# Optimization experiments

Hardware: AMD Instinct MI355X
Metric: run time of the kernel (lower is better)

Reference implementation:

```python
import jax, jax.numpy as jnp
import numpy as np

NUM_CLASSES = 4
SMOOTH = 1e-05
W_DICE, W_CE, W_BOUND = 1.0, 1.0, 0.01
BIG = 1e8  # effectively-infinite squared distance


def _edt_sq_pass(f, axis):
    # Exact 1D squared-distance transform along `axis` via min-plus:
    # out[i] = min_j f[j] + (i-j)^2  (brute-force O(n^2), fully vectorized)
    n = f.shape[axis]
    i = jnp.arange(n, dtype=f.dtype)
    d2 = (i[:, None] - i[None, :]) ** 2  # [n, n]
    fm = jnp.moveaxis(f, axis, -1)
    out = jnp.min(fm[..., None, :] + d2, axis=-1)
    return jnp.moveaxis(out, -1, axis)


def _edt(zero_mask):
    # Euclidean distance to the nearest True voxel of zero_mask
    # (equivalent to scipy distance_transform_edt(~zero_mask)'s convention:
    #  distance to nearest zero of the input == nearest True of zero_mask).
    f = jnp.where(zero_mask, 0.0, BIG).astype(jnp.float32)
    for ax in range(f.ndim):
        f = _edt_sq_pass(f, ax)
    return jnp.sqrt(f)


def _signed_distance(mask):
    # mask: bool [D,H,W]; signed distance map: + outside, - inside.
    d_out = _edt(mask)            # distance(1 - mask)
    d_in = _edt(~mask)            # distance(mask)
    sdf = d_out - d_in
    total = jnp.sum(mask)
    size = mask.size
    sdf = jnp.where(total == 0, jnp.ones_like(sdf), sdf)
    sdf = jnp.where(total == size, -jnp.ones_like(sdf), sdf)
    return sdf


def setup_inputs() -> dict:
    key = jax.random.key(0)
    k1, k2 = jax.random.split(key)
    preds = jax.random.normal(k1, (4, NUM_CLASSES, 64, 64, 64), dtype=jnp.float32)
    targets = jax.random.randint(k2, (4, 64, 64, 64), 0, NUM_CLASSES, dtype=jnp.int32)
    return {"preds": preds, "targets": targets}


def reference(preds, targets):
    B = preds.shape[0]
    probs = jax.nn.softmax(preds, axis=1)  # [B,C,D,H,W]

    # --- Soft Dice ---
    onehot = jax.nn.one_hot(targets, NUM_CLASSES, dtype=preds.dtype)  # [B,D,H,W,C]
    onehot = jnp.moveaxis(onehot, -1, 1)  # [B,C,D,H,W]
    inter = jnp.sum(probs * onehot, axis=(2, 3, 4))
    union = jnp.sum(probs, axis=(2, 3, 4)) + jnp.sum(onehot, axis=(2, 3, 4))
    dice = (2.0 * inter + SMOOTH) / (union + SMOOTH)
    l_dice = 1.0 - jnp.mean(dice)

    # --- Cross entropy (mean over all voxels) ---
    logp = jax.nn.log_softmax(preds, axis=1)
    picked = jnp.take_along_axis(logp, targets[:, None].astype(jnp.int32), axis=1)
    l_ce = -jnp.mean(picked)

    # --- Boundary loss (classes 1..C-1) ---
    l_bound = jnp.float32(0.0)
    for c in range(1, NUM_CLASSES):
        mask_c = targets == c  # [B,D,H,W]
        sdf_c = jax.vmap(_signed_distance)(mask_c)  # [B,D,H,W]
        l_bound = l_bound + jnp.sum(jnp.mean(sdf_c * probs[:, c], axis=(1, 2, 3)))
    l_bound = l_bound / (B * (NUM_CLASSES - 1))

    return W_DICE * l_dice + W_CE * l_ce + W_BOUND * l_bound
```

## Files before the change

kernel.cpp:

```cpp
#include <hip/hip_runtime.h>
#include <hip/hip_bf16.h>
#include <math.h>

#define NVOX 262144
#define BIGF 1e8f

__device__ __forceinline__ unsigned short f2bf(float x) {
    __hip_bfloat16 h = __float2bfloat16(x);
    return *reinterpret_cast<unsigned short*>(&h);
}
__device__ __forceinline__ float bf2f(unsigned short u) {
    __hip_bfloat16 h = *reinterpret_cast<__hip_bfloat16*>(&u);
    return __bfloat162float(h);
}
__device__ __forceinline__ unsigned short dist2_u16(unsigned long long mask, int w) {
    if (mask == 0ull) return 0xFFFFu;
    unsigned long long mr = mask >> w;
    unsigned long long ml = mask << (63 - w);
    int dr = mr ? __builtin_ctzll(mr) : 127;
    int dl = ml ? __builtin_clzll(ml) : 127;
    int dd = dr < dl ? dr : dl;
    return (unsigned short)(dd * dd);
}

__global__ __launch_bounds__(512) void k1_stats_edt1(
    const float* __restrict__ preds, const int* __restrict__ targets,
    unsigned short* __restrict__ bufA, unsigned short* __restrict__ probsT,
    float* __restrict__ part_stats) {
    __shared__ int tgt[64 * 65];
    __shared__ unsigned short tiles[3 * 64 * 65];
    __shared__ float sred[8 * 13];

    int blk = blockIdx.x;
    int b = blk >> 6, d = blk & 63;
    int t = threadIdx.x, lane = t & 63, wid = t >> 6;
    size_t tbase = (size_t)b * NVOX + (size_t)d * 4096;
    size_t pbase = (size_t)(b * 4) * NVOX + (size_t)d * 4096;

    float q[13];
    #pragma unroll
    for (int k = 0; k < 13; ++k) q[k] = 0.0f;

    for (int i = 0; i < 8; ++i) {
        int e = t + 512 * i;
        int h = e >> 6, w = e & 63;
        int tv = targets[tbase + e];
        tgt[h * 65 + w] = tv;
        float x0 = preds[pbase + e];
        float x1 = preds[pbase + NVOX + e];
        float x2 = preds[pbase + 2 * NVOX + e];
        float x3 = preds[pbase + 3 * NVOX + e];
        float m  = fmaxf(fmaxf(x0, x1), fmaxf(x2, x3));
        float e0 = expf(x0 - m), e1 = expf(x1 - m), e2 = expf(x2 - m), e3 = expf(x3 - m);
        float ssum = e0 + e1 + e2 + e3;
        float inv  = 1.0f / ssum;
        float p0 = e0 * inv, p1 = e1 * inv, p2 = e2 * inv, p3 = e3 * inv;
        float xt = (tv == 0) ? x0 : (tv == 1) ? x1 : (tv == 2) ? x2 : x3;
        q[12] += -(xt - m - logf(ssum));
        q[4] += p0; q[5] += p1; q[6] += p2; q[7] += p3;
        if (tv == 0)      { q[0] += p0; q[8]  += 1.0f; }
        else if (tv == 1) { q[1] += p1; q[9]  += 1.0f; }
        else if (tv == 2) { q[2] += p2; q[10] += 1.0f; }
        else              { q[3] += p3; q[11] += 1.0f; }
        int li = h * 65 + w;
        tiles[li]            = f2bf(p1);
        tiles[4160 + li]     = f2bf(p2);
        tiles[2 * 4160 + li] = f2bf(p3);
    }

    #pragma unroll
    for (int k = 0; k < 13; ++k) {
        float x = q[k];
        #pragma unroll
        for (int o = 32; o > 0; o >>= 1) x += __shfl_down(x, o);
        if (lane == 0) sred[wid * 13 + k] = x;
    }
    __syncthreads();
    if (t < 13) {
        float s = 0.0f;
        for (int j = 0; j < 8; ++j) s += sred[j * 13 + t];
        part_stats[t * 256 + blk] = s;
    }

    for (int c = 0; c < 3; ++c) {
        size_t obase = (size_t)(b * 3 + c) * NVOX + (size_t)d * 64;
        for (int w = wid; w < 64; w += 8)
            probsT[obase + (size_t)w * 4096 + lane] = tiles[c * 4160 + lane * 65 + w];
    }
    __syncthreads();

    unsigned short* tA = tiles;
    unsigned short* tB = tiles + 4160;
    for (int c = 1; c <= 3; ++c) {
        for (int r = 0; r < 8; ++r) {
            int row = wid * 8 + r;
            int tv = tgt[row * 65 + lane];
            unsigned long long mask = __ballot(tv == c);
            tA[row * 65 + lane] = dist2_u16(mask, lane);
            tB[row * 65 + lane] = dist2_u16(~mask, lane);
        }
        __syncthreads();
        int combo = b * 3 + c - 1;
        size_t oA = (size_t)combo * NVOX + (size_t)d * 64;
        size_t oB = (size_t)(combo + 12) * NVOX + (size_t)d * 64;
        for (int w = wid; w < 64; w += 8) {
            bufA[oA + (size_t)w * 4096 + lane] = tA[lane * 65 + w];
            bufA[oB + (size_t)w * 4096 + lane] = tB[lane * 65 + w];
        }
        __syncthreads();
    }
}

__global__ __launch_bounds__(512) void k2_edt23_sdf(
    const unsigned short* __restrict__ bufA, const unsigned short* __restrict__ probsT,
    float* __restrict__ part_bound) {
    __shared__ float pl[2][64 * 65];
    __shared__ float sredb[8];
    int blk = blockIdx.x;
    int combo = blk >> 6, w = blk & 63;
    int t = threadIdx.x, lane = t & 63, wid = t >> 6;

    for (int v = 0; v < 2; ++v) {
        const unsigned short* src = bufA + (size_t)(combo + 12 * v) * NVOX + (size_t)w * 4096;
        for (int i = 0; i < 8; ++i) {
            int e = t + 512 * i;
            unsigned short u = src[e];
            pl[v][e + (e >> 6)] = (u == 0xFFFFu) ? BIGF : (float)u;
        }
    }
    __syncthreads();

    for (int v = 0; v < 2; ++v) {
        for (int r = 0; r < 8; ++r) {
            int dd_ = wid * 8 + r;
            float* row = &pl[v][dd_ * 65];
            float best = row[lane];
            for (int dk = 1; dk < 64; ++dk) {
                float d2 = (float)(dk * dk);
                if (__all(d2 >= best)) break;
                int hl = lane - dk; hl = hl < 0 ? 0 : hl;
                int hr = lane + dk; hr = hr > 63 ? 63 : hr;
                best = fminf(fminf(best, row[hl] + d2), row[hr] + d2);
            }
            row[lane] = best;
        }
    }
    __syncthreads();
    for (int v = 0; v < 2; ++v) {
        for (int r = 0; r < 8; ++r) {
            int h = wid * 8 + r;
            float* col = &pl[v][h];
            float best = col[lane * 65];
            for (int dk = 1; dk < 64; ++dk) {
                float d2 = (float)(dk * dk);
                if (__all(d2 >= best)) break;
                int dl = lane - dk; dl = dl < 0 ? 0 : dl;
                int dr = lane + dk; dr = dr > 63 ? 63 : dr;
                best = fminf(fminf(best, col[dl * 65] + d2), col[dr * 65] + d2);
            }
            col[lane * 65] = best;
        }
    }
    __syncthreads();

    const unsigned short* pp = probsT + (size_t)combo * NVOX + (size_t)w * 4096;
    float acc = 0.0f;
    for (int i = 0; i < 8; ++i) {
        int e = t + 512 * i;
        int li = e + (e >> 6);
        float sdf = sqrtf(pl[0][li]) - sqrtf(pl[1][li]);
        acc += sdf * bf2f(pp[e]);
    }
    #pragma unroll
    for (int o = 32; o > 0; o >>= 1) acc += __shfl_down(acc, o);
    if (lane == 0) sredb[wid] = acc;
    __syncthreads();
    if (t == 0) {
        float s = 0.0f;
        for (int j = 0; j < 8; ++j) s += sredb[j];
        part_bound[blk] = s;
    }
}

__global__ __launch_bounds__(1024) void k3_final(
    const float* __restrict__ part_stats, const float* __restrict__ part_bound,
    float* __restrict__ out) {
    __shared__ double S[13 * 4];
    __shared__ double BND[12];
    int t = threadIdx.x, lane = t & 63, wid = t >> 6;

    if (t < 256) {
        for (int k = 0; k < 13; ++k) {
            float v = part_stats[k * 256 + t];
            #pragma unroll
            for (int o = 32; o > 0; o >>= 1) v += __shfl_down(v, o);
            if (lane == 0) S[k * 4 + wid] = (double)v;
        }
    }
    __syncthreads();
    if (t < 768) {
        float v = part_bound[t];
        #pragma unroll
        for (int o = 32; o > 0; o >>= 1) v += __shfl_down(v, o);
        if (lane == 0) BND[wid] = (double)v;
    }
    __syncthreads();
    if (t == 0) {
        const double NV = (double)NVOX;
        double dice_sum = 0.0;
        for (int b = 0; b < 4; ++b)
            for (int c = 0; c < 4; ++c) {
                double inter = S[c * 4 + b];
                double un    = S[(4 + c) * 4 + b] + S[(8 + c) * 4 + b];
                dice_sum += (2.0 * inter + 1e-5) / (un + 1e-5);
            }
        double l_dice = 1.0 - dice_sum / 16.0;
        double l_ce = (S[48] + S[49] + S[50] + S[51]) / (4.0 * NV);
        double lb = 0.0;
        for (int combo = 0; combo < 12; ++combo) {
            int b = combo / 3, c = combo % 3 + 1;
            double cnt = S[(8 + c) * 4 + b];
            double s;
            if (cnt == 0.0)      s =  S[(4 + c) * 4 + b];
            else if (cnt == NV)  s = -S[(4 + c) * 4 + b];
            else                 s =  BND[combo];
            lb += s / NV;
        }
        lb /= 12.0;
        out[0] = (float)(l_dice + l_ce + 0.01 * lb);
    }
}

extern "C" void kernel_launch(void* const* d_in, const int* in_sizes, int n_in,
                              void* d_out, int out_size, void* d_ws, size_t ws_size,
                              hipStream_t stream) {
    const float* preds   = (const float*)d_in[0];
    const int*   targets = (const int*)d_in[1];
    float* out = (float*)d_out;

    unsigned short* bufA   = (unsigned short*)d_ws;
    unsigned short* probsT = bufA + (size_t)24 * NVOX;
    float* part_stats = (float*)(probsT + (size_t)12 * NVOX);
    float* part_bound = part_stats + 13 * 256;

    k1_stats_edt1<<<256, 512, 0, stream>>>(preds, targets, bufA, probsT, part_stats);
    k2_edt23_sdf<<<768, 512, 0, stream>>>(bufA, probsT, part_bound);
    k3_final<<<1, 1024, 0, stream>>>(part_stats, part_bound, out);
}
```

Measured before the change: 51.49 us.

## Split stats and EDT passes into separate kernels, move second EDT pass earlier

Splits the old combined stats+first-pass kernel into a vectorized float4 softmax/stats kernel with 1024 blocks and a separate per-(b,d,class) kernel. The new kernel computes the W and H EDT passes in shared memory. The final kernel now does only the D pass plus the SDF reduction, and the stored intermediate layout is transposed accordingly. The aim is more parallelism and less serial work per block in the first stage. The cost is an extra kernel launch, rereading targets, and a changed final reduction layout.

```diff
diff --git a/kernel.cpp b/kernel.cpp
--- a/kernel.cpp
+++ b/kernel.cpp
@@ -23,49 +23,52 @@
     return (unsigned short)(dd * dd);
 }
 
-__global__ __launch_bounds__(512) void k1_stats_edt1(
+__global__ __launch_bounds__(256) void kA_stats_probs(
     const float* __restrict__ preds, const int* __restrict__ targets,
-    unsigned short* __restrict__ bufA, unsigned short* __restrict__ probsT,
-    float* __restrict__ part_stats) {
-    __shared__ int tgt[64 * 65];
-    __shared__ unsigned short tiles[3 * 64 * 65];
-    __shared__ float sred[8 * 13];
-
+    unsigned short* __restrict__ probsT, float* __restrict__ part_stats) {
+    __shared__ float sred[4 * 13];
     int blk = blockIdx.x;
-    int b = blk >> 6, d = blk & 63;
-    int t = threadIdx.x, lane = t & 63, wid = t >> 6;
-    size_t tbase = (size_t)b * NVOX + (size_t)d * 4096;
-    size_t pbase = (size_t)(b * 4) * NVOX + (size_t)d * 4096;
+    int b = blk >> 8, seg = blk & 255;
+    int t = threadIdx.x, lane = t & 63, wid = t >> 6;
+    size_t vbase = (size_t)seg * 1024 + 4 * t;
+    const float* p = preds + (size_t)(b * 4) * NVOX + vbase;
+    float4 x0 = *(const float4*)(p);
+    float4 x1 = *(const float4*)(p + NVOX);
+    float4 x2 = *(const float4*)(p + 2 * NVOX);
+    float4 x3 = *(const float4*)(p + 3 * NVOX);
+    int4 tv4 = *(const int4*)(targets + (size_t)b * NVOX + vbase);
 
     float q[13];
     #pragma unroll
     for (int k = 0; k < 13; ++k) q[k] = 0.0f;
-
-    for (int i = 0; i < 8; ++i) {
-        int e = t + 512 * i;
-        int h = e >> 6, w = e & 63;
-        int tv = targets[tbase + e];
-        tgt[h * 65 + w] = tv;
-        float x0 = preds[pbase + e];
-        float x1 = preds[pbase + NVOX + e];
-        float x2 = preds[pbase + 2 * NVOX + e];
-        float x3 = preds[pbase + 3 * NVOX + e];
-        float m  = fmaxf(fmaxf(x0, x1), fmaxf(x2, x3));
-        float e0 = expf(x0 - m), e1 = expf(x1 - m), e2 = expf(x2 - m), e3 = expf(x3 - m);
+    unsigned short pb[3][4];
+
+    #pragma unroll
+    for (int j = 0; j < 4; ++j) {
+        float a0 = (&x0.x)[j], a1 = (&x1.x)[j], a2 = (&x2.x)[j], a3 = (&x3.x)[j];
+        int tv = (&tv4.x)[j];
+        float m  = fmaxf(fmaxf(a0, a1), fmaxf(a2, a3));
+        float e0 = expf(a0 - m), e1 = expf(a1 - m), e2 = expf(a2 - m), e3 = expf(a3 - m);
         float ssum = e0 + e1 + e2 + e3;
         float inv  = 1.0f / ssum;
         float p0 = e0 * inv, p1 = e1 * inv, p2 = e2 * inv, p3 = e3 * inv;
-        float xt = (tv == 0) ? x0 : (tv == 1) ? x1 : (tv == 2) ? x2 : x3;
+        float xt = (tv == 0) ? a0 : (tv == 1) ? a1 : (tv == 2) ? a2 : a3;
         q[12] += -(xt - m - logf(ssum));
         q[4] += p0; q[5] += p1; q[6] += p2; q[7] += p3;
         if (tv == 0)      { q[0] += p0; q[8]  += 1.0f; }
         else if (tv == 1) { q[1] += p1; q[9]  += 1.0f; }
         else if (tv == 2) { q[2] += p2; q[10] += 1.0f; }
         else              { q[3] += p3; q[11] += 1.0f; }
-        int li = h * 65 + w;
-        tiles[li]            = f2bf(p1);
-        tiles[4160 + li]     = f2bf(p2);
-        tiles[2 * 4160 + li] = f2bf(p3);
+        pb[0][j] = f2bf(p1); pb[1][j] = f2bf(p2); pb[2][j] = f2bf(p3);
+    }
+
+    int v0 = (int)vbase;
+    int d = v0 >> 12, h = (v0 >> 6) & 63, w0 = v0 & 63;
+    size_t poff = (size_t)h * 4096 + d * 64 + w0;
+    #pragma unroll
+    for (int c = 0; c < 3; ++c) {
+        ushort4 u = make_ushort4(pb[c][0], pb[c][1], pb[c][2], pb[c][3]);
+        *(ushort4*)(probsT + (size_t)(b * 3 + c) * NVOX + poff) = u;
     }
 
     #pragma unroll
@@ -77,51 +80,89 @@
     }
     __syncthreads();
     if (t < 13) {
-        float s = 0.0f;
-        for (int j = 0; j < 8; ++j) s += sred[j * 13 + t];
-        part_stats[t * 256 + blk] = s;
-    }
-
-    for (int c = 0; c < 3; ++c) {
-        size_t obase = (size_t)(b * 3 + c) * NVOX + (size_t)d * 64;
-        for (int w = wid; w < 64; w += 8)
-            probsT[obase + (size_t)w * 4096 + lane] = tiles[c * 4160 + lane * 65 + w];
-    }
-    __syncthreads();
-
-    unsigned short* tA = tiles;
-    unsigned short* tB = tiles + 4160;
-    for (int c = 1; c <= 3; ++c) {
-        for (int r = 0; r < 8; ++r) {
-            int row = wid * 8 + r;
-            int tv = tgt[row * 65 + lane];
-            unsigned long long mask = __ballot(tv == c);
-            tA[row * 65 + lane] = dist2_u16(mask, lane);
-            tB[row * 65 + lane] = dist2_u16(~mask, lane);
-        }
-        __syncthreads();
-        int combo = b * 3 + c - 1;
-        size_t oA = (size_t)combo * NVOX + (size_t)d * 64;
-        size_t oB = (size_t)(combo + 12) * NVOX + (size_t)d * 64;
-        for (int w = wid; w < 64; w += 8) {
-            bufA[oA + (size_t)w * 4096 + lane] = tA[lane * 65 + w];
-            bufA[oB + (size_t)w * 4096 + lane] = tB[lane * 65 + w];
-        }
-        __syncthreads();
-    }
-}
-
-__global__ __launch_bounds__(512) void k2_edt23_sdf(
+        float s = sred[t] + sred[13 + t] + sred[26 + t] + sred[39 + t];
+        part_stats[t * 1024 + blk] = s;
+    }
+}
+
+__global__ __launch_bounds__(256) void kB_edt12(
+    const int* __restrict__ targets, unsigned short* __restrict__ bufA) {
+    __shared__ float tO[64 * 65];
+    __shared__ float tI[64 * 65];
+    int blk = blockIdx.x;
+    int cm = blk % 3;
+    int bd = blk / 3;
+    int d = bd & 63, b = bd >> 6;
+    int c = cm + 1;
+    int t = threadIdx.x, lane = t & 63, wid = t >> 6;
+    const int* tg = targets + (size_t)b * NVOX + (size_t)d * 4096;
+
+    #pragma unroll
+    for (int i = 0; i < 16; ++i) {
+        int e = t + 256 * i;
+        int h = wid + 4 * i;
+        int tv = tg[e];
+        unsigned long long mask = __ballot(tv == c);
+        unsigned short o  = dist2_u16(mask, lane);
+        unsigned short ii = dist2_u16(~mask, lane);
+        tO[h * 65 + lane] = (o  == 0xFFFFu) ? BIGF : (float)o;
+        tI[h * 65 + lane] = (ii == 0xFFFFu) ? BIGF : (float)ii;
+    }
+    __syncthreads();
+
+    float hf = (float)lane;
+    for (int r = 0; r < 16; ++r) {
+        int w = wid * 16 + r;
+        {
+            float best = tO[lane * 65 + w];
+            for (int dk = 1; dk < 64; ++dk) {
+                float d2 = (float)(dk * dk);
+                if (__all(d2 >= best)) break;
+                int hl = lane - dk; hl = hl < 0 ? 0 : hl;
+                int hr = lane + dk; hr = hr > 63 ? 63 : hr;
+                best = fminf(fminf(best, tO[hl * 65 + w] + d2), tO[hr * 65 + w] + d2);
+            }
+            tO[lane * 65 + w] = best;
+        }
+        {
+            float best = tI[lane * 65 + w];
+            for (int dk = 1; dk < 64; ++dk) {
+                float d2 = (float)(dk * dk);
+                if (__all(d2 >= best)) break;
+                int hl = lane - dk; hl = hl < 0 ? 0 : hl;
+                int hr = lane + dk; hr = hr > 63 ? 63 : hr;
+                best = fminf(fminf(best, tI[hl * 65 + w] + d2), tI[hr * 65 + w] + d2);
+            }
+            tI[lane * 65 + w] = best;
+        }
+    }
+    __syncthreads();
+
+    int combo = b * 3 + cm;
+    size_t oO = (size_t)combo * NVOX + (size_t)d * 64;
+    size_t oI = (size_t)(combo + 12) * NVOX + (size_t)d * 64;
+    #pragma unroll
+    for (int i = 0; i < 16; ++i) {
+        int h = wid + 4 * i;
+        float vo = tO[h * 65 + lane];
+        float vi = tI[h * 65 + lane];
+        bufA[oO + (size_t)h * 4096 + lane] = (vo >= 1e7f) ? 0xFFFFu : (unsigned short)vo;
+        bufA[oI + (size_t)h * 4096 + lane] = (vi >= 1e7f) ? 0xFFFFu : (unsigned short)vi;
+    }
+}
+
+__global__ __launch_bounds__(512) void k2_edt3_sdf(
     const unsigned short* __restrict__ bufA, const unsigned short* __restrict__ probsT,
     float* __restrict__ part_bound) {
     __shared__ float pl[2][64 * 65];
     __shared__ float sredb[8];
     int blk = blockIdx.x;
-    int combo = blk >> 6, w = blk & 63;
+    int combo = blk >> 6, h = blk & 63;
     int t = threadIdx.x, lane = t & 63, wid = t >> 6;
 
     for (int v = 0; v < 2; ++v) {
-        const unsigned short* src = bufA + (size_t)(combo + 12 * v) * NVOX + (size_t)w * 4096;
+        const unsigned short* src = bufA + (size_t)(combo + 12 * v) * NVOX + (size_t)h * 4096;
+        #pragma unroll
         for (int i = 0; i < 8; ++i) {
             int e = t + 512 * i;
             unsigned short u = src[e];
@@ -132,24 +173,8 @@
 
     for (int v = 0; v < 2; ++v) {
         for (int r = 0; r < 8; ++r) {
-            int dd_ = wid * 8 + r;
-            float* row = &pl[v][dd_ * 65];
-            float best = row[lane];
-            for (int dk = 1; dk < 64; ++dk) {
-                float d2 = (float)(dk * dk);
-                if (__all(d2 >= best)) break;
-                int hl = lane - dk; hl = hl < 0 ? 0 : hl;
-                int hr = lane + dk; hr = hr > 63 ? 63 : hr;
-                best = fminf(fminf(best, row[hl] + d2), row[hr] + d2);
-            }
-            row[lane] = best;
-        }
-    }
-    __syncthreads();
-    for (int v = 0; v < 2; ++v) {
-        for (int r = 0; r < 8; ++r) {
-            int h = wid * 8 + r;
-            float* col = &pl[v][h];
+            int w = wid * 8 + r;
+            float* col = &pl[v][w];
             float best = col[lane * 65];
             for (int dk = 1; dk < 64; ++dk) {
                 float d2 = (float)(dk * dk);
@@ -163,8 +188,9 @@
     }
     __syncthreads();
 
-    const unsigned short* pp = probsT + (size_t)combo * NVOX + (size_t)w * 4096;
+    const unsigned short* pp = probsT + (size_t)combo * NVOX + (size_t)h * 4096;
     float acc = 0.0f;
+    #pragma unroll
     for (int i = 0; i < 8; ++i) {
         int e = t + 512 * i;
         int li = e + (e >> 6);
@@ -185,19 +211,24 @@
 __global__ __launch_bounds__(1024) void k3_final(
     const float* __restrict__ part_stats, const float* __restrict__ part_bound,
     float* __restrict__ out) {
+    __shared__ float sred[13 * 16];
     __shared__ double S[13 * 4];
     __shared__ double BND[12];
     int t = threadIdx.x, lane = t & 63, wid = t >> 6;
 
-    if (t < 256) {
-        for (int k = 0; k < 13; ++k) {
-            float v = part_stats[k * 256 + t];
-            #pragma unroll
-            for (int o = 32; o > 0; o >>= 1) v += __shfl_down(v, o);
-            if (lane == 0) S[k * 4 + wid] = (double)v;
-        }
-    }
-    __syncthreads();
+    for (int k = 0; k < 13; ++k) {
+        float v = part_stats[k * 1024 + t];
+        #pragma unroll
+        for (int o = 32; o > 0; o >>= 1) v += __shfl_down(v, o);
+        if (lane == 0) sred[k * 16 + wid] = v;
+    }
+    __syncthreads();
+    if (t < 52) {
+        int k = t >> 2, b = t & 3;
+        double s = (double)sred[k * 16 + b * 4] + (double)sred[k * 16 + b * 4 + 1]
+                 + (double)sred[k * 16 + b * 4 + 2] + (double)sred[k * 16 + b * 4 + 3];
+        S[k * 4 + b] = s;
+    }
     if (t < 768) {
         float v = part_bound[t];
         #pragma unroll
@@ -241,9 +272,10 @@
     unsigned short* bufA   = (unsigned short*)d_ws;
     unsigned short* probsT = bufA + (size_t)24 * NVOX;
     float* part_stats = (float*)(probsT + (size_t)12 * NVOX);
-    float* part_bound = part_stats + 13 * 256;
-
-    k1_stats_edt1<<<256, 512, 0, stream>>>(preds, targets, bufA, probsT, part_stats);
-    k2_edt23_sdf<<<768, 512, 0, stream>>>(bufA, probsT, part_bound);
+    float* part_bound = part_stats + 13 * 1024;
+
+    kA_stats_probs<<<1024, 256, 0, stream>>>(preds, targets, probsT, part_stats);
+    kB_edt12<<<768, 256, 0, stream>>>(targets, bufA);
+    k2_edt3_sdf<<<768, 512, 0, stream>>>(bufA, probsT, part_bound);
     k3_final<<<1, 1024, 0, stream>>>(part_stats, part_bound, out);
 }
```

Result: slower. 55.81 us (+8.4%).
